# Kernel tuning notes

Measured on AMD Instinct MI355X. Metric: run time of the kernel, lower is better.

The kernel has to match this reference:

```python
import jax, jax.numpy as jnp
import numpy as np

N = 100000   # nodes
E = 1600000  # edges
EL = 200000  # decode pairs
D_IN, D_HID, D_OUT = 128, 128, 64


def setup_inputs() -> dict:
    key = jax.random.key(0)
    ks = jax.random.split(key, 9)
    x = jax.random.normal(ks[0], (N, D_IN), dtype=jnp.float32)
    edge_index = jax.random.randint(ks[1], (2, E), 0, N, dtype=jnp.int64)
    edge_label_index = jax.random.randint(ks[2], (2, EL), 0, N, dtype=jnp.int64)
    # GCNConv params: weight [in, out] (no bias inside linear), bias added after aggregation
    W1 = jax.random.normal(ks[3], (D_IN, D_HID), dtype=jnp.float32) / np.sqrt(D_IN)
    b1 = jnp.zeros((D_HID,), dtype=jnp.float32)
    W2 = jax.random.normal(ks[4], (D_HID, D_HID), dtype=jnp.float32) / np.sqrt(D_HID)
    b2 = jnp.zeros((D_HID,), dtype=jnp.float32)
    W3 = jax.random.normal(ks[5], (D_HID, D_OUT), dtype=jnp.float32) / np.sqrt(D_HID)
    b3 = jnp.zeros((D_OUT,), dtype=jnp.float32)
    return {"x": x, "edge_index": edge_index, "edge_label_index": edge_label_index,
            "W1": W1, "b1": b1, "W2": W2, "b2": b2, "W3": W3, "b3": b3}


def _gcn_norm(edge_index, num_nodes, dtype):
    # add self-loops, compute symmetric normalization deg^-1/2[src]*deg^-1/2[dst]
    loop = jnp.arange(num_nodes, dtype=edge_index.dtype)
    src = jnp.concatenate([edge_index[0], loop])
    dst = jnp.concatenate([edge_index[1], loop])
    deg = jax.ops.segment_sum(jnp.ones(src.shape, dtype=dtype), dst, num_segments=num_nodes)
    dinv = jax.lax.rsqrt(deg)  # deg >= 1 due to self-loops
    norm = dinv[src] * dinv[dst]
    return src, dst, norm


def _gcn_conv(h, W, b, src, dst, norm, num_nodes):
    h = h @ W                               # [N, out]
    msg = h[src] * norm[:, None]            # gather + scale  [E+N, out]
    out = jax.ops.segment_sum(msg, dst, num_segments=num_nodes)  # scatter-add
    return out + b


def reference(x, edge_index, edge_label_index, W1, b1, W2, b2, W3, b3):
    num_nodes = x.shape[0]
    src, dst, norm = _gcn_norm(edge_index, num_nodes, x.dtype)
    h = jax.nn.relu(_gcn_conv(x, W1, b1, src, dst, norm, num_nodes))
    h = jax.nn.relu(_gcn_conv(h, W2, b2, src, dst, norm, num_nodes))  # dropout is identity in eval
    z = _gcn_conv(h, W3, b3, src, dst, norm, num_nodes)
    # decode: dot product over candidate pairs
    return jnp.sum(z[edge_label_index[0]] * z[edge_label_index[1]], axis=-1)
```

## Files before the change

### kernel.cpp

```cpp
#include <hip/hip_runtime.h>
#include <hip/hip_bf16.h>

#define N_NODES 100000
#define N_EDGES 1600000
#define N_EL    200000

#define NBKT 782
#define NCHK 782
#define CHKE 2048
#define DCAP 2688
#define GT_GEMM ((N_NODES + 63) / 64)
#define GRID_FAT (3 * NCHK)

typedef unsigned int uint32;
typedef unsigned short ushort16;
typedef __attribute__((ext_vector_type(8))) short short8;
typedef __attribute__((ext_vector_type(4))) float f32x4;

static __device__ __forceinline__ ushort16 f2bf(float f) {
    uint32 u = __float_as_uint(f);
    u += 0x7fffu + ((u >> 16) & 1u);
    return (ushort16)(u >> 16);
}
static __device__ __forceinline__ float bf_lo(uint32 p) { return __uint_as_float(p << 16); }
static __device__ __forceinline__ float bf_hi(uint32 p) { return __uint_as_float(p & 0xffff0000u); }
static __device__ __forceinline__ uint32 pack2(float lo, float hi) {
    return (uint32)f2bf(lo) | ((uint32)f2bf(hi) << 16);
}

template <bool AT>
static __device__ __forceinline__ int scan782(const int* __restrict__ in,
                                              int* __restrict__ outv,
                                              int* s, int tid) {
    __syncthreads();
    int v[4]; int sum = 0;
    int i0 = tid * 4;
#pragma unroll
    for (int i = 0; i < 4; ++i) {
        int idx = i0 + i;
        int x = 0;
        if (idx < NBKT)
            x = AT ? __hip_atomic_load(&in[idx], __ATOMIC_ACQUIRE,
                                       __HIP_MEMORY_SCOPE_AGENT)
                   : in[idx];
        v[i] = x; sum += x;
    }
    s[tid] = sum;
    __syncthreads();
    for (int off = 1; off < 256; off <<= 1) {
        int u = (tid >= off) ? s[tid - off] : 0;
        __syncthreads();
        s[tid] += u;
        __syncthreads();
    }
    int excl = s[tid] - sum;
    int total = s[255];
    int run = excl;
#pragma unroll
    for (int i = 0; i < 4; ++i) {
        int idx = i0 + i;
        if (idx < NBKT) outv[idx] = run;
        run += v[i];
    }
    return total;
}

__global__ __launch_bounds__(256) void k_scanB(const int* __restrict__ H,
        int* __restrict__ CO, int* __restrict__ TT, int* __restrict__ BB,
        int* __restrict__ cnt) {
    __shared__ int s[256];
    __shared__ int lastflag;
    int b = blockIdx.x, tid = threadIdx.x;
    int total = scan782<false>(H + (size_t)b * NBKT, CO + (size_t)b * NBKT, s, tid);
    if (tid == 0) {
        __hip_atomic_store(&TT[b], total, __ATOMIC_RELEASE, __HIP_MEMORY_SCOPE_AGENT);
        int c = __hip_atomic_fetch_add(cnt, 1, __ATOMIC_ACQ_REL,
                                       __HIP_MEMORY_SCOPE_AGENT);
        lastflag = (c == NBKT - 1);
    }
    __syncthreads();
    if (!lastflag) return;
    int gt = scan782<true>(TT, BB, s, tid);
    __syncthreads();
    if (tid == 0) BB[NBKT] = gt;
}

__global__ __launch_bounds__(256) void k_csrC(const int* __restrict__ src,
        const int* __restrict__ dst, const int* __restrict__ CO,
        const int* __restrict__ BB, long long* __restrict__ ed) {
    __shared__ int cur[NBKT];
    int c = blockIdx.x, tid = threadIdx.x;
    for (int i = tid; i < NBKT; i += 256)
        cur[i] = BB[i] + CO[(size_t)i * NBKT + c];
    __syncthreads();
    int e0 = c * CHKE;
#pragma unroll
    for (int kk = 0; kk < 8; ++kk) {
        int e = e0 + kk * 256 + tid;
        if (e < N_EDGES) {
            int sE = src[e], dE = dst[e];
            int pos = atomicAdd(&cur[dE >> 7], 1);
            long long pv = (unsigned int)sE | ((long long)(unsigned int)dE << 32);
            __builtin_nontemporal_store(pv, &ed[pos]);
        }
    }
}

__global__ __launch_bounds__(256) void k_csrD(const long long* __restrict__ ed,
        const int* __restrict__ BB, int* __restrict__ rowptr,
        float* __restrict__ dinv, int* __restrict__ col, uint32* __restrict__ t32) {
    __shared__ long long eds[DCAP];
    __shared__ int deg[128], scn[128], cur[128];
    __shared__ float dv[128];
    int b = blockIdx.x, tid = threadIdx.x;
    int base = BB[b], lim = BB[b + 1];
    int n = lim - base;
    bool cached = (n <= DCAP);
    if (tid < 128) deg[tid] = 0;
    __syncthreads();
    for (int i = tid; i < n; i += 256) {
        long long e = ed[base + i];
        if (cached) eds[i] = e;
        int d = (int)(e >> 32);
        atomicAdd(&deg[d & 127], 1);
    }
    __syncthreads();
    if (tid < 128) scn[tid] = deg[tid];
    __syncthreads();
    for (int off = 1; off < 128; off <<= 1) {
        int u = 0;
        if (tid < 128 && tid >= off) u = scn[tid - off];
        __syncthreads();
        if (tid < 128) scn[tid] += u;
        __syncthreads();
    }
    if (tid < 128) {
        int excl = scn[tid] - deg[tid];
        cur[tid] = excl;
        int node = b * 128 + tid;
        if (node < N_NODES) {
            rowptr[node] = base + excl;
            float di = rsqrtf((float)(deg[tid] + 1));
            dinv[node] = di;
            dv[tid] = di;
        }
    }
    if (b == NBKT - 1 && tid == 0) rowptr[N_NODES] = BB[NBKT];
    __syncthreads();
    for (int i = tid; i < n; i += 256) {
        long long e = cached ? eds[i] : ed[base + i];
        int sE = (int)(e & 0xffffffff);
        int d = (int)(e >> 32);
        int p = atomicAdd(&cur[d & 127], 1);
        col[base + p] = sE;
    }
    __syncthreads();
    for (int idx = tid; idx < 128 * 64; idx += 256) {
        int ni = idx >> 6;
        int node = b * 128 + ni;
        if (node < N_NODES) {
            int k = idx & 63;
            size_t a = (size_t)node * 64 + k;
            uint32 p = t32[a];
            float di = dv[ni];
            t32[a] = pack2(bf_lo(p) * di, bf_hi(p) * di);
        }
    }
}

static __device__ __forceinline__ short8 load_afrag(const float* arow, int off) {
    float4 a0 = *(const float4*)(arow + off);
    float4 a1 = *(const float4*)(arow + off + 4);
    short8 af;
    af[0] = (short)f2bf(a0.x); af[1] = (short)f2bf(a0.y);
    af[2] = (short)f2bf(a0.z); af[3] = (short)f2bf(a0.w);
    af[4] = (short)f2bf(a1.x); af[5] = (short)f2bf(a1.y);
    af[6] = (short)f2bf(a1.z); af[7] = (short)f2bf(a1.w);
    return af;
}
static __device__ __forceinline__ short8 load_afrag(const ushort16* arow, int off) {
    return *(const short8*)(arow + off);
}

template <int D, typename AT, bool SCALE, int OS>
static __device__ __forceinline__ void gemm_body(int bid, const AT* __restrict__ A,
        const float* __restrict__ W, const float* __restrict__ dinv,
        ushort16* __restrict__ C, short* sB) {
    constexpr int NT = D / 16;
    constexpr int LNT = (NT == 8) ? 3 : 2;
    int tid = threadIdx.x;

    constexpr int COMBOS = 4 * 4 * NT * 16;
    for (int cc = tid; cc < COMBOS; cc += 256) {
        int nn = cc & 15;
        int nt = (cc >> 4) & (NT - 1);
        int q  = (cc >> (4 + LNT)) & 3;
        int kt = cc >> (6 + LNT);
        short8 pk;
#pragma unroll
        for (int j = 0; j < 8; ++j)
            pk[j] = (short)f2bf(W[(kt * 32 + q * 8 + j) * D + nt * 16 + nn]);
        *(short8*)&sB[(((kt * NT + nt) * 64) + q * 16 + nn) * 8] = pk;
    }
    __syncthreads();

    int w = tid >> 6;
    int l = tid & 63;
    int q = l >> 4;
    int nn15 = l & 15;
    int m0 = bid * 64 + w * 16;

    f32x4 acc[NT];
#pragma unroll
    for (int i = 0; i < NT; ++i) acc[i] = (f32x4){0.f, 0.f, 0.f, 0.f};

    int m = m0 + nn15;
    m = min(m, N_NODES - 1);
    const AT* arow = A + (size_t)m * 128;

#pragma unroll
    for (int kt = 0; kt < 4; ++kt) {
        short8 af = load_afrag(arow, kt * 32 + q * 8);
#pragma unroll
        for (int nt = 0; nt < NT; ++nt) {
            short8 bf = *(const short8*)&sB[((kt * NT + nt) * 64 + l) * 8];
            acc[nt] = __builtin_amdgcn_mfma_f32_16x16x32_bf16(af, bf, acc[nt], 0, 0, 0);
        }
    }

    float4 dvv;
    if constexpr (SCALE) dvv = *(const float4*)(dinv + m0 + 4 * q);
    const float* dvp = (const float*)&dvv;
#pragma unroll
    for (int nt = 0; nt < NT; ++nt) {
#pragma unroll
        for (int r = 0; r < 4; ++r) {
            int node = m0 + q * 4 + r;
            if (node < N_NODES) {
                float val = acc[nt][r];
                if constexpr (SCALE) val *= dvp[r];
                C[(size_t)node * OS + nt * 16 + nn15] = f2bf(val);
            }
        }
    }
}

template <int D, typename AT, bool SCALE, int OS>
__global__ __launch_bounds__(256, 5) void k_gemm_mfma(const AT* __restrict__ A,
        const float* __restrict__ W, const float* __restrict__ dinv,
        ushort16* __restrict__ C) {
    __shared__ short sB[4 * (D / 16) * 64 * 8];
    gemm_body<D, AT, SCALE, OS>(blockIdx.x, A, W, dinv, C, sB);
}

__global__ __launch_bounds__(256, 5) void k_fat1(const float* __restrict__ A,
        const float* __restrict__ W, ushort16* __restrict__ C,
        const int* __restrict__ dst, int* __restrict__ H) {
    __shared__ __align__(16) char smem[32768];
    unsigned bid = blockIdx.x;
    unsigned g = bid / 3u;
    unsigned rem = bid - g * 3u;
    int tid = threadIdx.x;
    if (rem < 2u) {
        unsigned gid = g * 2u + rem;
        if (gid < GT_GEMM)
            gemm_body<128, float, false, 128>(gid, A, W, nullptr, C, (short*)smem);
    } else {
        int* hist = (int*)smem;
        for (int i = tid; i < NBKT; i += 256) hist[i] = 0;
        __syncthreads();
        int e0 = (int)g * CHKE;
#pragma unroll
        for (int kk = 0; kk < 8; ++kk) {
            int e = e0 + kk * 256 + tid;
            if (e < N_EDGES) atomicAdd(&hist[dst[e] >> 7], 1);
        }
        __syncthreads();
        for (int i = tid; i < NBKT; i += 256)
            H[(size_t)i * NBKT + g] = hist[i];
    }
}

template <bool RELU>
__global__ void k_gather128(const int* __restrict__ rowptr, const int* __restrict__ col,
                            const float* __restrict__ dinv, const uint32* __restrict__ t,
                            const float* __restrict__ b, uint32* __restrict__ outbuf) {
    __shared__ int sc[4][64];
    int tid = threadIdx.x;
    unsigned wid = (blockIdx.x * 256u + tid) >> 6;
    if (wid >= N_NODES) return;
    int w = tid >> 6;
    int lane = tid & 63;
    int h = lane >> 5;
    int k = lane & 31;
    int beg = rowptr[wid], end = rowptr[wid + 1];
    float a0 = 0.f, a1 = 0.f, a2 = 0.f, a3 = 0.f;
    if (h == 0) {
        uint2 p = ((const uint2*)(t + (size_t)wid * 64))[k];
        a0 = bf_lo(p.x); a1 = bf_hi(p.x); a2 = bf_lo(p.y); a3 = bf_hi(p.y);
    }
    for (int base = beg; base < end; base += 64) {
        int cnt = min(end - base, 64);
        int c = N_NODES;
        if (lane < cnt) c = col[base + lane];
        sc[w][lane] = c;
        int nb = (cnt + 7) >> 3;
        for (int j8 = 0; j8 < nb; ++j8) {
            int j = j8 << 3;
            int r0 = sc[w][j + 0 + h];
            int r1 = sc[w][j + 2 + h];
            int r2 = sc[w][j + 4 + h];
            int r3 = sc[w][j + 6 + h];
            uint2 v0 = ((const uint2*)(t + (size_t)r0 * 64))[k];
            uint2 v1 = ((const uint2*)(t + (size_t)r1 * 64))[k];
            uint2 v2 = ((const uint2*)(t + (size_t)r2 * 64))[k];
            uint2 v3 = ((const uint2*)(t + (size_t)r3 * 64))[k];
            a0 += (bf_lo(v0.x) + bf_lo(v1.x)) + (bf_lo(v2.x) + bf_lo(v3.x));
            a1 += (bf_hi(v0.x) + bf_hi(v1.x)) + (bf_hi(v2.x) + bf_hi(v3.x));
            a2 += (bf_lo(v0.y) + bf_lo(v1.y)) + (bf_lo(v2.y) + bf_lo(v3.y));
            a3 += (bf_hi(v0.y) + bf_hi(v1.y)) + (bf_hi(v2.y) + bf_hi(v3.y));
        }
    }
    a0 += __shfl_xor(a0, 32);
    a1 += __shfl_xor(a1, 32);
    a2 += __shfl_xor(a2, 32);
    a3 += __shfl_xor(a3, 32);
    if (h == 0) {
        float di = dinv[wid];
        float4 bb = ((const float4*)b)[k];
        float o0 = fmaf(di, a0, bb.x);
        float o1 = fmaf(di, a1, bb.y);
        float o2 = fmaf(di, a2, bb.z);
        float o3 = fmaf(di, a3, bb.w);
        if (RELU) {
            o0 = fmaxf(o0, 0.f); o1 = fmaxf(o1, 0.f);
            o2 = fmaxf(o2, 0.f); o3 = fmaxf(o3, 0.f);
        }
        unsigned long long pv = (unsigned long long)pack2(o0, o1)
                              | ((unsigned long long)pack2(o2, o3) << 32);
        __builtin_nontemporal_store(pv,
            (unsigned long long*)(outbuf + (size_t)wid * 64) + k);
    }
}

__global__ void k_gather64(const int* __restrict__ rowptr, const int* __restrict__ col,
                           const float* __restrict__ dinv, const uint32* __restrict__ t,
                           const float* __restrict__ b, uint32* __restrict__ outbuf) {
    __shared__ int sc[4][64];
    int tid = threadIdx.x;
    unsigned wid = (blockIdx.x * 256u + tid) >> 6;
    if (wid >= N_NODES) return;
    int w = tid >> 6;
    int lane = tid & 63;
    int h = lane >> 4;
    int k = lane & 15;
    int beg = rowptr[wid], end = rowptr[wid + 1];
    float a0 = 0.f, a1 = 0.f, a2 = 0.f, a3 = 0.f;
    if (h == 0) {
        uint2 p = ((const uint2*)(t + (size_t)wid * 64))[k];
        a0 = bf_lo(p.x); a1 = bf_hi(p.x); a2 = bf_lo(p.y); a3 = bf_hi(p.y);
    }
    for (int base = beg; base < end; base += 64) {
        int cnt = min(end - base, 64);
        int c = N_NODES;
        if (lane < cnt) c = col[base + lane];
        sc[w][lane] = c;
        int nb = (cnt + 7) >> 3;
        for (int j8 = 0; j8 < nb; ++j8) {
            int j = j8 << 3;
            int r0 = sc[w][j + h];
            int r1 = sc[w][j + 4 + h];
            uint2 v0 = ((const uint2*)(t + (size_t)r0 * 64))[k];
            uint2 v1 = ((const uint2*)(t + (size_t)r1 * 64))[k];
            a0 += bf_lo(v0.x) + bf_lo(v1.x);
            a1 += bf_hi(v0.x) + bf_hi(v1.x);
            a2 += bf_lo(v0.y) + bf_lo(v1.y);
            a3 += bf_hi(v0.y) + bf_hi(v1.y);
        }
    }
    a0 += __shfl_xor(a0, 16); a0 += __shfl_xor(a0, 32);
    a1 += __shfl_xor(a1, 16); a1 += __shfl_xor(a1, 32);
    a2 += __shfl_xor(a2, 16); a2 += __shfl_xor(a2, 32);
    a3 += __shfl_xor(a3, 16); a3 += __shfl_xor(a3, 32);
    if (h == 0) {
        float di = dinv[wid];
        float4 bb = ((const float4*)b)[k];
        float o0 = fmaf(di, a0, bb.x);
        float o1 = fmaf(di, a1, bb.y);
        float o2 = fmaf(di, a2, bb.z);
        float o3 = fmaf(di, a3, bb.w);
        unsigned long long pv = (unsigned long long)pack2(o0, o1)
                              | ((unsigned long long)pack2(o2, o3) << 32);
        __builtin_nontemporal_store(pv,
            (unsigned long long*)(outbuf + (size_t)wid * 32) + k);
    }
}

__global__ void k_decode(const int* __restrict__ eli, const ushort16* __restrict__ z,
                         float* __restrict__ out) {
    int e = blockIdx.x * blockDim.x + threadIdx.x;
    if (e >= N_EL) return;
    int a = eli[e];
    int b = eli[N_EL + e];
    const uint4* za = (const uint4*)(z + (size_t)a * 64);
    const uint4* zb = (const uint4*)(z + (size_t)b * 64);
    float acc = 0.0f;
#pragma unroll
    for (int i = 0; i < 8; ++i) {
        uint4 va = za[i], vb = zb[i];
        acc += bf_lo(va.x) * bf_lo(vb.x) + bf_hi(va.x) * bf_hi(vb.x);
        acc += bf_lo(va.y) * bf_lo(vb.y) + bf_hi(va.y) * bf_hi(vb.y);
        acc += bf_lo(va.z) * bf_lo(vb.z) + bf_hi(va.z) * bf_hi(vb.z);
        acc += bf_lo(va.w) * bf_lo(vb.w) + bf_hi(va.w) * bf_hi(vb.w);
    }
    out[e] = acc;
}

extern "C" void kernel_launch(void* const* d_in, const int* in_sizes, int n_in,
                              void* d_out, int out_size, void* d_ws, size_t ws_size,
                              hipStream_t stream) {
    const float* x   = (const float*)d_in[0];
    const int*   ei  = (const int*)d_in[1];
    const int*   eli = (const int*)d_in[2];
    const float* W1  = (const float*)d_in[3];
    const float* b1  = (const float*)d_in[4];
    const float* W2  = (const float*)d_in[5];
    const float* b2  = (const float*)d_in[6];
    const float* W3  = (const float*)d_in[7];
    const float* b3  = (const float*)d_in[8];
    float* out = (float*)d_out;

    const int* srcA = ei;
    const int* dstA = ei + N_EDGES;

    char* ws = (char*)d_ws;
    float*      dinv   = (float*)    (ws + 0);
    int*        rowptr = (int*)      (ws + (1024u << 10));
    int*        TT     = (int*)      (ws + (1536u << 10));
    int*        BB     = (int*)      (ws + (1638u << 10));
    int*        cnt    = (int*)      (ws + (1792u << 10));
    int*        col    = (int*)      (ws + (2048u << 10));
    int*        H      = (int*)      (ws + (9u << 20));
    int*        CO     = (int*)      (ws + (12u << 20));
    long long*  ed     = (long long*)(ws + (16u << 20));
    ushort16*   t      = (ushort16*) (ws + (32u << 20));
    ushort16*   aggb   = (ushort16*) (ws + (60u << 20));

    const int B = 256;
    const int gG  = (N_NODES * 64 + B - 1) / B;
    const int gEL = (N_EL + B - 1) / B;

    hipMemsetAsync(cnt, 0, 4, stream);
    hipMemsetAsync((char*)t + (size_t)N_NODES * 256, 0, 256, stream);

    k_fat1<<<GRID_FAT, B, 0, stream>>>(x, W1, t, dstA, H);
    k_scanB<<<NBKT, B, 0, stream>>>(H, CO, TT, BB, cnt);
    k_csrC<<<NCHK, B, 0, stream>>>(srcA, dstA, CO, BB, ed);
    k_csrD<<<NBKT, B, 0, stream>>>(ed, BB, rowptr, dinv, col, (uint32*)t);

    k_gather128<true><<<gG, B, 0, stream>>>(rowptr, col, dinv, (const uint32*)t,
                                            b1, (uint32*)aggb);
    k_gemm_mfma<128, ushort16, true, 128><<<GT_GEMM, B, 0, stream>>>(aggb, W2, dinv, t);
    k_gather128<true><<<gG, B, 0, stream>>>(rowptr, col, dinv, (const uint32*)t,
                                            b2, (uint32*)aggb);
    k_gemm_mfma<64, ushort16, true, 128><<<GT_GEMM, B, 0, stream>>>(aggb, W3, dinv, t);
    k_gather64<<<gG, B, 0, stream>>>(rowptr, col, dinv, (const uint32*)t, b3,
                                     (uint32*)aggb);

    k_decode<<<gEL, B, 0, stream>>>(eli, aggb, out);
}
```

Baseline: 461.7 us.

## Fuse whole GCN pipeline into one persistent kernel with grid barriers

Replaces the ten-kernel sequence with a single persistent kernel of 1024 blocks that moves between phases through atomic-counter grid barriers. CSR construction changes from a bucketed histogram, scan and scatter to per-node atomic counting with a recorded rank, a two-level scan and a direct scatter of col. The aim is to remove launch overheads and tail gaps between the many small kernels. In exchange it needs all 1024 blocks co-resident to avoid deadlock, the gathers now run on a grid-stride loop, and the nontemporal stores were dropped.

```diff
diff --git a/kernel.cpp b/kernel.cpp
--- a/kernel.cpp
+++ b/kernel.cpp
@@ -5,12 +5,9 @@
 #define N_EDGES 1600000
 #define N_EL    200000
 
-#define NBKT 782
-#define NCHK 782
-#define CHKE 2048
-#define DCAP 2688
+#define NB2 ((N_NODES + 511) / 512)
 #define GT_GEMM ((N_NODES + 63) / 64)
-#define GRID_FAT (3 * NCHK)
+#define GRIDN 1024
 
 typedef unsigned int uint32;
 typedef unsigned short ushort16;
@@ -28,144 +25,15 @@
     return (uint32)f2bf(lo) | ((uint32)f2bf(hi) << 16);
 }
 
-template <bool AT>
-static __device__ __forceinline__ int scan782(const int* __restrict__ in,
-                                              int* __restrict__ outv,
-                                              int* s, int tid) {
+static __device__ __forceinline__ void gsync(int* cbar, int phase, int tid) {
     __syncthreads();
-    int v[4]; int sum = 0;
-    int i0 = tid * 4;
-#pragma unroll
-    for (int i = 0; i < 4; ++i) {
-        int idx = i0 + i;
-        int x = 0;
-        if (idx < NBKT)
-            x = AT ? __hip_atomic_load(&in[idx], __ATOMIC_ACQUIRE,
-                                       __HIP_MEMORY_SCOPE_AGENT)
-                   : in[idx];
-        v[i] = x; sum += x;
-    }
-    s[tid] = sum;
+    if (tid == 0) {
+        __hip_atomic_fetch_add(cbar, 1, __ATOMIC_ACQ_REL, __HIP_MEMORY_SCOPE_AGENT);
+        while (__hip_atomic_load(cbar, __ATOMIC_ACQUIRE, __HIP_MEMORY_SCOPE_AGENT)
+               < phase * GRIDN)
+            __builtin_amdgcn_s_sleep(8);
+    }
     __syncthreads();
-    for (int off = 1; off < 256; off <<= 1) {
-        int u = (tid >= off) ? s[tid - off] : 0;
-        __syncthreads();
-        s[tid] += u;
-        __syncthreads();
-    }
-    int excl = s[tid] - sum;
-    int total = s[255];
-    int run = excl;
-#pragma unroll
-    for (int i = 0; i < 4; ++i) {
-        int idx = i0 + i;
-        if (idx < NBKT) outv[idx] = run;
-        run += v[i];
-    }
-    return total;
-}
-
-__global__ __launch_bounds__(256) void k_scanB(const int* __restrict__ H,
-        int* __restrict__ CO, int* __restrict__ TT, int* __restrict__ BB,
-        int* __restrict__ cnt) {
-    __shared__ int s[256];
-    __shared__ int lastflag;
-    int b = blockIdx.x, tid = threadIdx.x;
-    int total = scan782<false>(H + (size_t)b * NBKT, CO + (size_t)b * NBKT, s, tid);
-    if (tid == 0) {
-        __hip_atomic_store(&TT[b], total, __ATOMIC_RELEASE, __HIP_MEMORY_SCOPE_AGENT);
-        int c = __hip_atomic_fetch_add(cnt, 1, __ATOMIC_ACQ_REL,
-                                       __HIP_MEMORY_SCOPE_AGENT);
-        lastflag = (c == NBKT - 1);
-    }
-    __syncthreads();
-    if (!lastflag) return;
-    int gt = scan782<true>(TT, BB, s, tid);
-    __syncthreads();
-    if (tid == 0) BB[NBKT] = gt;
-}
-
-__global__ __launch_bounds__(256) void k_csrC(const int* __restrict__ src,
-        const int* __restrict__ dst, const int* __restrict__ CO,
-        const int* __restrict__ BB, long long* __restrict__ ed) {
-    __shared__ int cur[NBKT];
-    int c = blockIdx.x, tid = threadIdx.x;
-    for (int i = tid; i < NBKT; i += 256)
-        cur[i] = BB[i] + CO[(size_t)i * NBKT + c];
-    __syncthreads();
-    int e0 = c * CHKE;
-#pragma unroll
-    for (int kk = 0; kk < 8; ++kk) {
-        int e = e0 + kk * 256 + tid;
-        if (e < N_EDGES) {
-            int sE = src[e], dE = dst[e];
-            int pos = atomicAdd(&cur[dE >> 7], 1);
-            long long pv = (unsigned int)sE | ((long long)(unsigned int)dE << 32);
-            __builtin_nontemporal_store(pv, &ed[pos]);
-        }
-    }
-}
-
-__global__ __launch_bounds__(256) void k_csrD(const long long* __restrict__ ed,
-        const int* __restrict__ BB, int* __restrict__ rowptr,
-        float* __restrict__ dinv, int* __restrict__ col, uint32* __restrict__ t32) {
-    __shared__ long long eds[DCAP];
-    __shared__ int deg[128], scn[128], cur[128];
-    __shared__ float dv[128];
-    int b = blockIdx.x, tid = threadIdx.x;
-    int base = BB[b], lim = BB[b + 1];
-    int n = lim - base;
-    bool cached = (n <= DCAP);
-    if (tid < 128) deg[tid] = 0;
-    __syncthreads();
-    for (int i = tid; i < n; i += 256) {
-        long long e = ed[base + i];
-        if (cached) eds[i] = e;
-        int d = (int)(e >> 32);
-        atomicAdd(&deg[d & 127], 1);
-    }
-    __syncthreads();
-    if (tid < 128) scn[tid] = deg[tid];
-    __syncthreads();
-    for (int off = 1; off < 128; off <<= 1) {
-        int u = 0;
-        if (tid < 128 && tid >= off) u = scn[tid - off];
-        __syncthreads();
-        if (tid < 128) scn[tid] += u;
-        __syncthreads();
-    }
-    if (tid < 128) {
-        int excl = scn[tid] - deg[tid];
-        cur[tid] = excl;
-        int node = b * 128 + tid;
-        if (node < N_NODES) {
-            rowptr[node] = base + excl;
-            float di = rsqrtf((float)(deg[tid] + 1));
-            dinv[node] = di;
-            dv[tid] = di;
-        }
-    }
-    if (b == NBKT - 1 && tid == 0) rowptr[N_NODES] = BB[NBKT];
-    __syncthreads();
-    for (int i = tid; i < n; i += 256) {
-        long long e = cached ? eds[i] : ed[base + i];
-        int sE = (int)(e & 0xffffffff);
-        int d = (int)(e >> 32);
-        int p = atomicAdd(&cur[d & 127], 1);
-        col[base + p] = sE;
-    }
-    __syncthreads();
-    for (int idx = tid; idx < 128 * 64; idx += 256) {
-        int ni = idx >> 6;
-        int node = b * 128 + ni;
-        if (node < N_NODES) {
-            int k = idx & 63;
-            size_t a = (size_t)node * 64 + k;
-            uint32 p = t32[a];
-            float di = dv[ni];
-            t32[a] = pack2(bf_lo(p) * di, bf_hi(p) * di);
-        }
-    }
 }
 
 static __device__ __forceinline__ short8 load_afrag(const float* arow, int off) {
@@ -189,6 +57,7 @@
     constexpr int NT = D / 16;
     constexpr int LNT = (NT == 8) ? 3 : 2;
     int tid = threadIdx.x;
+    __syncthreads();
 
     constexpr int COMBOS = 4 * 4 * NT * 16;
     for (int cc = tid; cc < COMBOS; cc += 256) {
@@ -234,186 +103,274 @@
 #pragma unroll
     for (int nt = 0; nt < NT; ++nt) {
 #pragma unroll
-        for (int r = 0; r < 4; ++r) {
-            int node = m0 + q * 4 + r;
+        for (int rr = 0; rr < 4; ++rr) {
+            int node = m0 + q * 4 + rr;
             if (node < N_NODES) {
-                float val = acc[nt][r];
-                if constexpr (SCALE) val *= dvp[r];
+                float val = acc[nt][rr];
+                if constexpr (SCALE) val *= dvp[rr];
                 C[(size_t)node * OS + nt * 16 + nn15] = f2bf(val);
             }
         }
     }
 }
 
-template <int D, typename AT, bool SCALE, int OS>
-__global__ __launch_bounds__(256, 5) void k_gemm_mfma(const AT* __restrict__ A,
-        const float* __restrict__ W, const float* __restrict__ dinv,
-        ushort16* __restrict__ C) {
-    __shared__ short sB[4 * (D / 16) * 64 * 8];
-    gemm_body<D, AT, SCALE, OS>(blockIdx.x, A, W, dinv, C, sB);
-}
-
-__global__ __launch_bounds__(256, 5) void k_fat1(const float* __restrict__ A,
-        const float* __restrict__ W, ushort16* __restrict__ C,
-        const int* __restrict__ dst, int* __restrict__ H) {
-    __shared__ __align__(16) char smem[32768];
-    unsigned bid = blockIdx.x;
-    unsigned g = bid / 3u;
-    unsigned rem = bid - g * 3u;
-    int tid = threadIdx.x;
-    if (rem < 2u) {
-        unsigned gid = g * 2u + rem;
-        if (gid < GT_GEMM)
-            gemm_body<128, float, false, 128>(gid, A, W, nullptr, C, (short*)smem);
-    } else {
-        int* hist = (int*)smem;
-        for (int i = tid; i < NBKT; i += 256) hist[i] = 0;
-        __syncthreads();
-        int e0 = (int)g * CHKE;
-#pragma unroll
-        for (int kk = 0; kk < 8; ++kk) {
-            int e = e0 + kk * 256 + tid;
-            if (e < N_EDGES) atomicAdd(&hist[dst[e] >> 7], 1);
-        }
-        __syncthreads();
-        for (int i = tid; i < NBKT; i += 256)
-            H[(size_t)i * NBKT + g] = hist[i];
-    }
-}
-
 template <bool RELU>
-__global__ void k_gather128(const int* __restrict__ rowptr, const int* __restrict__ col,
-                            const float* __restrict__ dinv, const uint32* __restrict__ t,
-                            const float* __restrict__ b, uint32* __restrict__ outbuf) {
-    __shared__ int sc[4][64];
-    int tid = threadIdx.x;
-    unsigned wid = (blockIdx.x * 256u + tid) >> 6;
-    if (wid >= N_NODES) return;
+static __device__ __forceinline__ void gather128_phase(const int* __restrict__ rowptr,
+        const int* __restrict__ col, const float* __restrict__ dinv,
+        const uint32* __restrict__ t, const float* __restrict__ b,
+        uint32* __restrict__ outbuf, int bid, int tid, void* smem) {
+    int (*sc)[64] = (int(*)[64])smem;
     int w = tid >> 6;
     int lane = tid & 63;
     int h = lane >> 5;
     int k = lane & 31;
-    int beg = rowptr[wid], end = rowptr[wid + 1];
-    float a0 = 0.f, a1 = 0.f, a2 = 0.f, a3 = 0.f;
-    if (h == 0) {
-        uint2 p = ((const uint2*)(t + (size_t)wid * 64))[k];
-        a0 = bf_lo(p.x); a1 = bf_hi(p.x); a2 = bf_lo(p.y); a3 = bf_hi(p.y);
-    }
-    for (int base = beg; base < end; base += 64) {
-        int cnt = min(end - base, 64);
-        int c = N_NODES;
-        if (lane < cnt) c = col[base + lane];
-        sc[w][lane] = c;
-        int nb = (cnt + 7) >> 3;
-        for (int j8 = 0; j8 < nb; ++j8) {
-            int j = j8 << 3;
-            int r0 = sc[w][j + 0 + h];
-            int r1 = sc[w][j + 2 + h];
-            int r2 = sc[w][j + 4 + h];
-            int r3 = sc[w][j + 6 + h];
-            uint2 v0 = ((const uint2*)(t + (size_t)r0 * 64))[k];
-            uint2 v1 = ((const uint2*)(t + (size_t)r1 * 64))[k];
-            uint2 v2 = ((const uint2*)(t + (size_t)r2 * 64))[k];
-            uint2 v3 = ((const uint2*)(t + (size_t)r3 * 64))[k];
-            a0 += (bf_lo(v0.x) + bf_lo(v1.x)) + (bf_lo(v2.x) + bf_lo(v3.x));
-            a1 += (bf_hi(v0.x) + bf_hi(v1.x)) + (bf_hi(v2.x) + bf_hi(v3.x));
-            a2 += (bf_lo(v0.y) + bf_lo(v1.y)) + (bf_lo(v2.y) + bf_lo(v3.y));
-            a3 += (bf_hi(v0.y) + bf_hi(v1.y)) + (bf_hi(v2.y) + bf_hi(v3.y));
-        }
-    }
-    a0 += __shfl_xor(a0, 32);
-    a1 += __shfl_xor(a1, 32);
-    a2 += __shfl_xor(a2, 32);
-    a3 += __shfl_xor(a3, 32);
-    if (h == 0) {
-        float di = dinv[wid];
-        float4 bb = ((const float4*)b)[k];
-        float o0 = fmaf(di, a0, bb.x);
-        float o1 = fmaf(di, a1, bb.y);
-        float o2 = fmaf(di, a2, bb.z);
-        float o3 = fmaf(di, a3, bb.w);
-        if (RELU) {
-            o0 = fmaxf(o0, 0.f); o1 = fmaxf(o1, 0.f);
-            o2 = fmaxf(o2, 0.f); o3 = fmaxf(o3, 0.f);
-        }
-        unsigned long long pv = (unsigned long long)pack2(o0, o1)
-                              | ((unsigned long long)pack2(o2, o3) << 32);
-        __builtin_nontemporal_store(pv,
-            (unsigned long long*)(outbuf + (size_t)wid * 64) + k);
-    }
-}
-
-__global__ void k_gather64(const int* __restrict__ rowptr, const int* __restrict__ col,
-                           const float* __restrict__ dinv, const uint32* __restrict__ t,
-                           const float* __restrict__ b, uint32* __restrict__ outbuf) {
-    __shared__ int sc[4][64];
-    int tid = threadIdx.x;
-    unsigned wid = (blockIdx.x * 256u + tid) >> 6;
-    if (wid >= N_NODES) return;
+    for (int wid = bid * 4 + w; wid < N_NODES; wid += GRIDN * 4) {
+        int beg = rowptr[wid], end = rowptr[wid + 1];
+        float a0 = 0.f, a1 = 0.f, a2 = 0.f, a3 = 0.f;
+        if (h == 0) {
+            uint2 p = ((const uint2*)(t + (size_t)wid * 64))[k];
+            a0 = bf_lo(p.x); a1 = bf_hi(p.x); a2 = bf_lo(p.y); a3 = bf_hi(p.y);
+        }
+        for (int base = beg; base < end; base += 64) {
+            int cnt = min(end - base, 64);
+            int c = N_NODES;
+            if (lane < cnt) c = col[base + lane];
+            sc[w][lane] = c;
+            int nb8 = (cnt + 7) >> 3;
+            for (int j8 = 0; j8 < nb8; ++j8) {
+                int j = j8 << 3;
+                int r0 = sc[w][j + 0 + h];
+                int r1 = sc[w][j + 2 + h];
+                int r2 = sc[w][j + 4 + h];
+                int r3 = sc[w][j + 6 + h];
+                uint2 v0 = ((const uint2*)(t + (size_t)r0 * 64))[k];
+                uint2 v1 = ((const uint2*)(t + (size_t)r1 * 64))[k];
+                uint2 v2 = ((const uint2*)(t + (size_t)r2 * 64))[k];
+                uint2 v3 = ((const uint2*)(t + (size_t)r3 * 64))[k];
+                a0 += (bf_lo(v0.x) + bf_lo(v1.x)) + (bf_lo(v2.x) + bf_lo(v3.x));
+                a1 += (bf_hi(v0.x) + bf_hi(v1.x)) + (bf_hi(v2.x) + bf_hi(v3.x));
+                a2 += (bf_lo(v0.y) + bf_lo(v1.y)) + (bf_lo(v2.y) + bf_lo(v3.y));
+                a3 += (bf_hi(v0.y) + bf_hi(v1.y)) + (bf_hi(v2.y) + bf_hi(v3.y));
+            }
+        }
+        a0 += __shfl_xor(a0, 32);
+        a1 += __shfl_xor(a1, 32);
+        a2 += __shfl_xor(a2, 32);
+        a3 += __shfl_xor(a3, 32);
+        if (h == 0) {
+            float di = dinv[wid];
+            float4 bb = ((const float4*)b)[k];
+            float o0 = fmaf(di, a0, bb.x);
+            float o1 = fmaf(di, a1, bb.y);
+            float o2 = fmaf(di, a2, bb.z);
+            float o3 = fmaf(di, a3, bb.w);
+            if (RELU) {
+                o0 = fmaxf(o0, 0.f); o1 = fmaxf(o1, 0.f);
+                o2 = fmaxf(o2, 0.f); o3 = fmaxf(o3, 0.f);
+            }
+            unsigned long long pv = (unsigned long long)pack2(o0, o1)
+                                  | ((unsigned long long)pack2(o2, o3) << 32);
+            *((unsigned long long*)(outbuf + (size_t)wid * 64) + k) = pv;
+        }
+    }
+}
+
+static __device__ __forceinline__ void gather64_phase(const int* __restrict__ rowptr,
+        const int* __restrict__ col, const float* __restrict__ dinv,
+        const uint32* __restrict__ z, const float* __restrict__ b,
+        uint32* __restrict__ outbuf, int bid, int tid, void* smem) {
+    int (*sc)[64] = (int(*)[64])smem;
     int w = tid >> 6;
     int lane = tid & 63;
     int h = lane >> 4;
     int k = lane & 15;
-    int beg = rowptr[wid], end = rowptr[wid + 1];
-    float a0 = 0.f, a1 = 0.f, a2 = 0.f, a3 = 0.f;
-    if (h == 0) {
-        uint2 p = ((const uint2*)(t + (size_t)wid * 64))[k];
-        a0 = bf_lo(p.x); a1 = bf_hi(p.x); a2 = bf_lo(p.y); a3 = bf_hi(p.y);
-    }
-    for (int base = beg; base < end; base += 64) {
-        int cnt = min(end - base, 64);
-        int c = N_NODES;
-        if (lane < cnt) c = col[base + lane];
-        sc[w][lane] = c;
-        int nb = (cnt + 7) >> 3;
-        for (int j8 = 0; j8 < nb; ++j8) {
-            int j = j8 << 3;
-            int r0 = sc[w][j + h];
-            int r1 = sc[w][j + 4 + h];
-            uint2 v0 = ((const uint2*)(t + (size_t)r0 * 64))[k];
-            uint2 v1 = ((const uint2*)(t + (size_t)r1 * 64))[k];
-            a0 += bf_lo(v0.x) + bf_lo(v1.x);
-            a1 += bf_hi(v0.x) + bf_hi(v1.x);
-            a2 += bf_lo(v0.y) + bf_lo(v1.y);
-            a3 += bf_hi(v0.y) + bf_hi(v1.y);
-        }
-    }
-    a0 += __shfl_xor(a0, 16); a0 += __shfl_xor(a0, 32);
-    a1 += __shfl_xor(a1, 16); a1 += __shfl_xor(a1, 32);
-    a2 += __shfl_xor(a2, 16); a2 += __shfl_xor(a2, 32);
-    a3 += __shfl_xor(a3, 16); a3 += __shfl_xor(a3, 32);
-    if (h == 0) {
-        float di = dinv[wid];
-        float4 bb = ((const float4*)b)[k];
-        float o0 = fmaf(di, a0, bb.x);
-        float o1 = fmaf(di, a1, bb.y);
-        float o2 = fmaf(di, a2, bb.z);
-        float o3 = fmaf(di, a3, bb.w);
-        unsigned long long pv = (unsigned long long)pack2(o0, o1)
-                              | ((unsigned long long)pack2(o2, o3) << 32);
-        __builtin_nontemporal_store(pv,
-            (unsigned long long*)(outbuf + (size_t)wid * 32) + k);
-    }
-}
-
-__global__ void k_decode(const int* __restrict__ eli, const ushort16* __restrict__ z,
-                         float* __restrict__ out) {
-    int e = blockIdx.x * blockDim.x + threadIdx.x;
-    if (e >= N_EL) return;
-    int a = eli[e];
-    int b = eli[N_EL + e];
-    const uint4* za = (const uint4*)(z + (size_t)a * 64);
-    const uint4* zb = (const uint4*)(z + (size_t)b * 64);
-    float acc = 0.0f;
-#pragma unroll
-    for (int i = 0; i < 8; ++i) {
-        uint4 va = za[i], vb = zb[i];
-        acc += bf_lo(va.x) * bf_lo(vb.x) + bf_hi(va.x) * bf_hi(vb.x);
-        acc += bf_lo(va.y) * bf_lo(vb.y) + bf_hi(va.y) * bf_hi(vb.y);
-        acc += bf_lo(va.z) * bf_lo(vb.z) + bf_hi(va.z) * bf_hi(vb.z);
-        acc += bf_lo(va.w) * bf_lo(vb.w) + bf_hi(va.w) * bf_hi(vb.w);
-    }
-    out[e] = acc;
+    for (int wid = bid * 4 + w; wid < N_NODES; wid += GRIDN * 4) {
+        int beg = rowptr[wid], end = rowptr[wid + 1];
+        float a0 = 0.f, a1 = 0.f, a2 = 0.f, a3 = 0.f;
+        if (h == 0) {
+            uint2 p = ((const uint2*)(z + (size_t)wid * 32))[k];
+            a0 = bf_lo(p.x); a1 = bf_hi(p.x); a2 = bf_lo(p.y); a3 = bf_hi(p.y);
+        }
+        for (int base = beg; base < end; base += 64) {
+            int cnt = min(end - base, 64);
+            int c = N_NODES;
+            if (lane < cnt) c = col[base + lane];
+            sc[w][lane] = c;
+            int nb8 = (cnt + 7) >> 3;
+            for (int j8 = 0; j8 < nb8; ++j8) {
+                int j = j8 << 3;
+                int r0 = sc[w][j + h];
+                int r1 = sc[w][j + 4 + h];
+                uint2 v0 = ((const uint2*)(z + (size_t)r0 * 32))[k];
+                uint2 v1 = ((const uint2*)(z + (size_t)r1 * 32))[k];
+                a0 += bf_lo(v0.x) + bf_lo(v1.x);
+                a1 += bf_hi(v0.x) + bf_hi(v1.x);
+                a2 += bf_lo(v0.y) + bf_lo(v1.y);
+                a3 += bf_hi(v0.y) + bf_hi(v1.y);
+            }
+        }
+        a0 += __shfl_xor(a0, 16); a0 += __shfl_xor(a0, 32);
+        a1 += __shfl_xor(a1, 16); a1 += __shfl_xor(a1, 32);
+        a2 += __shfl_xor(a2, 16); a2 += __shfl_xor(a2, 32);
+        a3 += __shfl_xor(a3, 16); a3 += __shfl_xor(a3, 32);
+        if (h == 0) {
+            float di = dinv[wid];
+            float4 bb = ((const float4*)b)[k];
+            float o0 = fmaf(di, a0, bb.x);
+            float o1 = fmaf(di, a1, bb.y);
+            float o2 = fmaf(di, a2, bb.z);
+            float o3 = fmaf(di, a3, bb.w);
+            unsigned long long pv = (unsigned long long)pack2(o0, o1)
+                                  | ((unsigned long long)pack2(o2, o3) << 32);
+            *((unsigned long long*)(outbuf + (size_t)wid * 32) + k) = pv;
+        }
+    }
+}
+
+__global__ __launch_bounds__(256, 4) void k_mega(
+    const float* __restrict__ x, const int* __restrict__ ei,
+    const int* __restrict__ eli,
+    const float* __restrict__ W1, const float* __restrict__ b1,
+    const float* __restrict__ W2, const float* __restrict__ b2,
+    const float* __restrict__ W3, const float* __restrict__ b3,
+    float* __restrict__ out,
+    float* __restrict__ dinv, int* __restrict__ lrp, int* __restrict__ rowptr,
+    int* __restrict__ bsum, int* __restrict__ cpad, int* __restrict__ cbar,
+    int* __restrict__ col, int* __restrict__ r,
+    ushort16* __restrict__ t, ushort16* __restrict__ aggb)
+{
+    __shared__ __align__(16) char smem[32768];
+    const int tid = threadIdx.x;
+    const int bid = blockIdx.x;
+    const int* srcA = ei;
+    const int* dstA = ei + N_EDGES;
+    uint32* t32 = (uint32*)t;
+
+    for (int task = bid; task < 2346; task += GRIDN) {
+        int rem = task % 3;
+        if (rem < 2) {
+            int gid = (task / 3) * 2 + rem;
+            if (gid < GT_GEMM)
+                gemm_body<128, float, false, 128>(gid, x, W1, nullptr, t,
+                                                  (short*)smem);
+        } else {
+            int g = task / 3;
+            int e0 = g * 2048 + tid;
+            int d[8], rv[8];
+#pragma unroll
+            for (int kk = 0; kk < 8; ++kk) {
+                int e = e0 + kk * 256;
+                if (e < N_EDGES) d[kk] = dstA[e];
+            }
+#pragma unroll
+            for (int kk = 0; kk < 8; ++kk) {
+                int e = e0 + kk * 256;
+                if (e < N_EDGES) rv[kk] = atomicAdd(&cpad[d[kk]], 1);
+            }
+#pragma unroll
+            for (int kk = 0; kk < 8; ++kk) {
+                int e = e0 + kk * 256;
+                if (e < N_EDGES) r[e] = rv[kk];
+            }
+        }
+    }
+    gsync(cbar, 1, tid);
+
+    if (bid < NB2) {
+        int* s = (int*)smem;
+        int c = bid;
+        int n0 = c * 512 + tid * 2;
+        int va = (n0     < N_NODES) ? cpad[n0]     : 0;
+        int vb = (n0 + 1 < N_NODES) ? cpad[n0 + 1] : 0;
+        int sum2 = va + vb;
+        s[tid] = sum2;
+        __syncthreads();
+        for (int off = 1; off < 256; off <<= 1) {
+            int u = (tid >= off) ? s[tid - off] : 0;
+            __syncthreads();
+            s[tid] += u;
+            __syncthreads();
+        }
+        int excl = s[tid] - sum2;
+        if (n0 <= N_NODES) {
+            lrp[n0] = excl;
+            if (n0 < N_NODES) dinv[n0] = rsqrtf((float)(va + 1));
+        }
+        if (n0 + 1 <= N_NODES) {
+            lrp[n0 + 1] = excl + va;
+            if (n0 + 1 < N_NODES) dinv[n0 + 1] = rsqrtf((float)(vb + 1));
+        }
+        if (tid == 255) bsum[c] = s[255];
+    }
+    if (bid == GRIDN - 1 && tid < 64)
+        t32[(size_t)N_NODES * 64 + tid] = 0;
+    gsync(cbar, 2, tid);
+
+    {
+        int* s = (int*)smem;
+        int* sboff = (int*)smem + 288;
+        int v = (tid < NB2) ? bsum[tid] : 0;
+        s[tid] = v;
+        __syncthreads();
+        for (int off = 1; off < 256; off <<= 1) {
+            int u = (tid >= off) ? s[tid - off] : 0;
+            __syncthreads();
+            s[tid] += u;
+            __syncthreads();
+        }
+        if (tid < NB2) sboff[tid] = s[tid] - v;
+        __syncthreads();
+        for (int i = bid * 256 + tid; i <= N_NODES; i += GRIDN * 256)
+            rowptr[i] = lrp[i] + sboff[i >> 9];
+        for (int e = bid * 256 + tid; e < N_EDGES; e += GRIDN * 256) {
+            int dd = dstA[e];
+            col[lrp[dd] + sboff[dd >> 9] + r[e]] = srcA[e];
+        }
+        for (int idx = bid * 256 + tid; idx < N_NODES * 64; idx += GRIDN * 256) {
+            int node = idx >> 6;
+            uint32 p = t32[idx];
+            float di = dinv[node];
+            t32[idx] = pack2(bf_lo(p) * di, bf_hi(p) * di);
+        }
+    }
+    gsync(cbar, 3, tid);
+
+    gather128_phase<true>(rowptr, col, dinv, t32, b1, (uint32*)aggb, bid, tid, smem);
+    gsync(cbar, 4, tid);
+
+    for (int gid = bid; gid < GT_GEMM; gid += GRIDN)
+        gemm_body<128, ushort16, true, 128>(gid, aggb, W2, dinv, t, (short*)smem);
+    gsync(cbar, 5, tid);
+
+    gather128_phase<true>(rowptr, col, dinv, t32, b2, (uint32*)aggb, bid, tid, smem);
+    gsync(cbar, 6, tid);
+
+    if (bid == GRIDN - 1 && tid < 32)
+        t32[(size_t)N_NODES * 32 + tid] = 0;
+    for (int gid = bid; gid < GT_GEMM; gid += GRIDN)
+        gemm_body<64, ushort16, true, 64>(gid, aggb, W3, dinv, t, (short*)smem);
+    gsync(cbar, 7, tid);
+
+    gather64_phase(rowptr, col, dinv, t32, b3, (uint32*)aggb, bid, tid, smem);
+    gsync(cbar, 8, tid);
+
+    const ushort16* z = (const ushort16*)aggb;
+    for (int e = bid * 256 + tid; e < N_EL; e += GRIDN * 256) {
+        int a = eli[e];
+        int bnd = eli[N_EL + e];
+        const uint4* za = (const uint4*)(z + (size_t)a * 64);
+        const uint4* zb = (const uint4*)(z + (size_t)bnd * 64);
+        float acc = 0.0f;
+#pragma unroll
+        for (int i = 0; i < 8; ++i) {
+            uint4 va = za[i], vb = zb[i];
+            acc += bf_lo(va.x) * bf_lo(vb.x) + bf_hi(va.x) * bf_hi(vb.x);
+            acc += bf_lo(va.y) * bf_lo(vb.y) + bf_hi(va.y) * bf_hi(vb.y);
+            acc += bf_lo(va.z) * bf_lo(vb.z) + bf_hi(va.z) * bf_hi(vb.z);
+            acc += bf_lo(va.w) * bf_lo(vb.w) + bf_hi(va.w) * bf_hi(vb.w);
+        }
+        out[e] = acc;
+    }
 }
 
 extern "C" void kernel_launch(void* const* d_in, const int* in_sizes, int n_in,
@@ -430,42 +387,20 @@
     const float* b3  = (const float*)d_in[8];
     float* out = (float*)d_out;
 
-    const int* srcA = ei;
-    const int* dstA = ei + N_EDGES;
-
     char* ws = (char*)d_ws;
-    float*      dinv   = (float*)    (ws + 0);
-    int*        rowptr = (int*)      (ws + (1024u << 10));
-    int*        TT     = (int*)      (ws + (1536u << 10));
-    int*        BB     = (int*)      (ws + (1638u << 10));
-    int*        cnt    = (int*)      (ws + (1792u << 10));
-    int*        col    = (int*)      (ws + (2048u << 10));
-    int*        H      = (int*)      (ws + (9u << 20));
-    int*        CO     = (int*)      (ws + (12u << 20));
-    long long*  ed     = (long long*)(ws + (16u << 20));
-    ushort16*   t      = (ushort16*) (ws + (32u << 20));
-    ushort16*   aggb   = (ushort16*) (ws + (60u << 20));
-
-    const int B = 256;
-    const int gG  = (N_NODES * 64 + B - 1) / B;
-    const int gEL = (N_EL + B - 1) / B;
-
-    hipMemsetAsync(cnt, 0, 4, stream);
-    hipMemsetAsync((char*)t + (size_t)N_NODES * 256, 0, 256, stream);
-
-    k_fat1<<<GRID_FAT, B, 0, stream>>>(x, W1, t, dstA, H);
-    k_scanB<<<NBKT, B, 0, stream>>>(H, CO, TT, BB, cnt);
-    k_csrC<<<NCHK, B, 0, stream>>>(srcA, dstA, CO, BB, ed);
-    k_csrD<<<NBKT, B, 0, stream>>>(ed, BB, rowptr, dinv, col, (uint32*)t);
-
-    k_gather128<true><<<gG, B, 0, stream>>>(rowptr, col, dinv, (const uint32*)t,
-                                            b1, (uint32*)aggb);
-    k_gemm_mfma<128, ushort16, true, 128><<<GT_GEMM, B, 0, stream>>>(aggb, W2, dinv, t);
-    k_gather128<true><<<gG, B, 0, stream>>>(rowptr, col, dinv, (const uint32*)t,
-                                            b2, (uint32*)aggb);
-    k_gemm_mfma<64, ushort16, true, 128><<<GT_GEMM, B, 0, stream>>>(aggb, W3, dinv, t);
-    k_gather64<<<gG, B, 0, stream>>>(rowptr, col, dinv, (const uint32*)t, b3,
-                                     (uint32*)aggb);
-
-    k_decode<<<gEL, B, 0, stream>>>(eli, aggb, out);
-}
+    float*    dinv   = (float*)   (ws + 0);
+    int*      lrp    = (int*)     (ws + (1024u << 10));
+    int*      rowptr = (int*)     (ws + (1536u << 10));
+    int*      bsum   = (int*)     (ws + (2007u << 10));
+    int*      cpad   = (int*)     (ws + (2048u << 10));
+    int*      col    = (int*)     (ws + (3072u << 10));
+    int*      r      = (int*)     (ws + (10u << 20));
+    ushort16* t      = (ushort16*)(ws + (20u << 20));
+    ushort16* aggb   = (ushort16*)(ws + (48u << 20));
+    int*      cbar   = cpad + N_NODES;
+
+    hipMemsetAsync(cpad, 0, ((size_t)N_NODES + 1) * sizeof(int), stream);
+    k_mega<<<GRIDN, 256, 0, stream>>>(x, ei, eli, W1, b1, W2, b2, W3, b3, out,
+                                      dinv, lrp, rowptr, bsum, cpad, cbar,
+                                      col, r, t, aggb);
+}
```

Measured after the change: 1.691 ms. +266.3%, slower.
